# Kernel tuning notes

Measured on AMD Instinct MI355X. Metric: run time of the kernel, lower is better.

## Reference

```python
import jax, jax.numpy as jnp
import numpy as np

DIM = 256
HEADS = 8
HD = DIM // HEADS        # head_dim = 32
WS = 8                   # window_size (Wh = Ww = 8)
NEXP = 8                 # num_experts
HID = 128                # attr_hidden_size (router hidden)
SCALE = HD ** -0.5


def _window_partition(x, ws):
    # (B, H, W, C) -> (B * H//ws * W//ws, ws, ws, C)
    B, H, W, C = x.shape
    x = x.reshape(B, H // ws, ws, W // ws, ws, C)
    return x.transpose(0, 1, 3, 2, 4, 5).reshape(-1, ws, ws, C)


def _window_reverse(w, ws, B, H, W):
    # inverse of _window_partition
    C = w.shape[-1]
    x = w.reshape(B, H // ws, W // ws, ws, ws, C)
    return x.transpose(0, 1, 3, 2, 4, 5).reshape(B, H, W, C)


def _rope2(x):
    # 2D rotary embedding over a window: x (B*, Wh, Ww, d).
    # First d/2 channels rotated by row position, last d/2 by column position.
    B, Wh, Ww, d = x.shape
    d2 = d // 2

    def angles(L, dd):
        inv = 1.0 / (10000.0 ** (jnp.arange(0, dd, 2, dtype=jnp.float32) / dd))
        return jnp.arange(L, dtype=jnp.float32)[:, None] * inv[None, :]  # (L, dd//2)

    def rotate(v, ang, bshape):
        # v: (B, Wh, Ww, dd) pairs interleaved; ang broadcast as bshape
        p = v.reshape(*v.shape[:-1], -1, 2)
        c = jnp.cos(ang).reshape(bshape)
        s = jnp.sin(ang).reshape(bshape)
        o0 = p[..., 0] * c - p[..., 1] * s
        o1 = p[..., 0] * s + p[..., 1] * c
        return jnp.stack([o0, o1], axis=-1).reshape(v.shape)

    ah = angles(Wh, d2)  # (Wh, d2//2)
    aw = angles(Ww, d2)  # (Ww, d2//2)
    xh = rotate(x[..., :d2], ah, (1, Wh, 1, d2 // 2))
    xw = rotate(x[..., d2:], aw, (1, 1, Ww, d2 // 2))
    return jnp.concatenate([xh, xw], axis=-1)


def _moe_linear(xf, routes, w, b):
    # Top-1 dispatch: per-expert dense GEMM, masked select (jit-safe, static shapes).
    # xf: (T, in), routes: (T,) int, w: (E, out, in), b: (E, out)
    out = jnp.zeros((xf.shape[0], w.shape[1]), xf.dtype)
    for i in range(w.shape[0]):
        y = xf @ w[i].T + b[i]
        out = jnp.where((routes == i)[:, None], y, out)
    return out


def setup_inputs() -> dict:
    key = jax.random.key(0)
    ks = jax.random.split(key, 8)
    sc = 0.02
    return {
        "x": jax.random.normal(ks[0], (8, 64, 64, DIM), jnp.float32),
        "router_w1": jax.random.normal(ks[1], (HID, DIM), jnp.float32) * sc,
        "router_b1": jnp.zeros((HID,), jnp.float32),
        "router_w2": jax.random.normal(ks[2], (NEXP, HID), jnp.float32) * sc,
        "router_b2": jnp.zeros((NEXP,), jnp.float32),
        "qkv_w": jax.random.normal(ks[3], (NEXP, 3 * DIM, DIM), jnp.float32) * sc,
        "qkv_b": jnp.zeros((NEXP, 3 * DIM), jnp.float32),
        "proj_w": jax.random.normal(ks[4], (NEXP, DIM, DIM), jnp.float32) * sc,
        "proj_b": jnp.zeros((NEXP, DIM), jnp.float32),
    }


def reference(x, router_w1, router_b1, router_w2, router_b2,
              qkv_w, qkv_b, proj_w, proj_b):
    Bs, H, W, C = x.shape
    xf = x.reshape(-1, C)  # (T, C), T = Bs*H*W

    # --- Top-1 router (eval mode: no noise, no token dropping) ---
    h = jax.nn.relu(xf @ router_w1.T + router_b1)
    router_logits = h @ router_w2.T + router_b2          # (T, E)
    router_probs = jax.nn.softmax(router_logits, axis=-1)
    route_prob_max = jnp.max(router_probs, axis=-1)       # (T,)
    routes = jnp.argmax(router_probs, axis=-1)            # (T,)

    # --- per-expert QKV projection (grouped dispatch) ---
    qkv = _moe_linear(xf, routes, qkv_w, qkv_b)           # (T, 3C)
    qkv = qkv.reshape(Bs, H, W, 3 * C)

    # --- window partition (shift=0, dilated=1 -> no roll, mask=None) ---
    qw = _window_partition(qkv, WS).reshape(-1, WS * WS, 3 * C)
    B_, N, _ = qw.shape
    qkv5 = qw.reshape(B_, N, 3, HEADS, HD).transpose(2, 0, 3, 1, 4)  # (3,B_,h,N,hd)
    q, k, v = qkv5[0], qkv5[1], qkv5[2]

    # --- RoPE on q, k over the 2D window ---
    q = _rope2(q.reshape(-1, WS, WS, HD)).reshape(B_, HEADS, N, HD)
    k = _rope2(k.reshape(-1, WS, WS, HD)).reshape(B_, HEADS, N, HD)

    # --- windowed attention (moe_mask is all zeros in eval: no drops) ---
    attn = jax.nn.softmax((q * SCALE) @ k.swapaxes(-2, -1), axis=-1)  # (B_,h,N,N)
    out = (attn @ v).swapaxes(1, 2).reshape(B_, N, C)

    # --- window reverse ---
    out = _window_reverse(out.reshape(-1, WS, WS, C), WS, Bs, H, W)

    # --- per-expert output projection + Switch-style prob scaling ---
    of = _moe_linear(out.reshape(-1, C), routes, proj_w, proj_b)
    of = of * route_prob_max[:, None]
    return of.reshape(Bs, H, W, C)
```

## Files before the change

kernel.cpp:

```cpp
#include <hip/hip_runtime.h>
#include <hip/hip_bf16.h>

typedef unsigned short u16;
typedef unsigned int u32;
typedef __attribute__((ext_vector_type(8))) short short8;
typedef __attribute__((ext_vector_type(4))) float f32x4;

#define T_TOK 32768
#define SCALE_ATT 0.17677669529663687f

__device__ __forceinline__ u16 f2bf(float f){
  u32 u = __float_as_uint(f);
  u32 r = u + 0x7fffu + ((u >> 16) & 1u);
  return (u16)(r >> 16);
}
__device__ __forceinline__ float bf2f(u16 h){
  return __uint_as_float(((u32)h) << 16);
}

__global__ void k_cvt(const float* __restrict__ s, u16* __restrict__ d, int n4){
  int i = blockIdx.x * blockDim.x + threadIdx.x;
  if (i < n4){
    float4 v = ((const float4*)s)[i];
    ushort4 o;
    o.x = f2bf(v.x); o.y = f2bf(v.y); o.z = f2bf(v.z); o.w = f2bf(v.w);
    ((ushort4*)d)[i] = o;
  }
}

__global__ void k_cvt_split(const float* __restrict__ s, u16* __restrict__ hi,
                            u16* __restrict__ lo, int n){
  int i = blockIdx.x * blockDim.x + threadIdx.x;
  if (i < n){
    float v = s[i];
    u16 h = f2bf(v);
    hi[i] = h;
    lo[i] = f2bf(v - bf2f(h));
  }
}

__global__ void k_init(int* counts, int* cursors){
  int t = threadIdx.x;
  if (t < 8){ counts[t] = 0; cursors[t] = 0; }
}

__global__ __launch_bounds__(256) void k_router(
    const float* __restrict__ x, const u16* __restrict__ w1h, const u16* __restrict__ w1l,
    const float* __restrict__ b1, const float* __restrict__ w2, const float* __restrict__ b2,
    int* __restrict__ routes, float* __restrict__ pmax, int* __restrict__ counts,
    u16* __restrict__ x_bf)
{
  __shared__ __align__(16) char smem[64*132*4];
  u16* Ah = (u16*)smem;
  u16* Al = Ah + 2560;
  u16* Bh = Al + 2560;
  u16* Bl = Bh + 5120;
  float* Hs = (float*)smem;
  __shared__ int lhist[8];

  int tid = threadIdx.x;
  int t0 = blockIdx.x * 64;
  int wv = tid >> 6, lane = tid & 63, quad = lane >> 4, l16 = lane & 15;
  if (tid < 8) lhist[tid] = 0;

  int arow = tid >> 2, acg = tid & 3;
  int brow = tid >> 1, bhalf = tid & 1;

  f32x4 acc[4][2];
  #pragma unroll
  for (int i = 0; i < 4; ++i)
    #pragma unroll
    for (int j = 0; j < 2; ++j)
      #pragma unroll
      for (int rr = 0; rr < 4; ++rr) acc[i][j][rr] = 0.f;

  for (int kt = 0; kt < 8; ++kt){
    const float* gx = x + (size_t)(t0 + arow) * 256 + kt * 32 + acg * 8;
    float4 v0 = *(const float4*)gx;
    float4 v1 = *(const float4*)(gx + 4);
    ushort4 h0, h1, l0, l1;
    h0.x = f2bf(v0.x); h0.y = f2bf(v0.y); h0.z = f2bf(v0.z); h0.w = f2bf(v0.w);
    h1.x = f2bf(v1.x); h1.y = f2bf(v1.y); h1.z = f2bf(v1.z); h1.w = f2bf(v1.w);
    l0.x = f2bf(v0.x - bf2f(h0.x)); l0.y = f2bf(v0.y - bf2f(h0.y));
    l0.z = f2bf(v0.z - bf2f(h0.z)); l0.w = f2bf(v0.w - bf2f(h0.w));
    l1.x = f2bf(v1.x - bf2f(h1.x)); l1.y = f2bf(v1.y - bf2f(h1.y));
    l1.z = f2bf(v1.z - bf2f(h1.z)); l1.w = f2bf(v1.w - bf2f(h1.w));
    u16* gxb = x_bf + (size_t)(t0 + arow) * 256 + kt * 32 + acg * 8;
    *(ushort4*)gxb = h0; *(ushort4*)(gxb + 4) = h1;
    const u16* gwh = w1h + (size_t)brow * 256 + kt * 32 + bhalf * 16;
    const u16* gwl = w1l + (size_t)brow * 256 + kt * 32 + bhalf * 16;
    uint4 wh0 = *(const uint4*)gwh;
    uint4 wh1 = *(const uint4*)(gwh + 8);
    uint4 wl0 = *(const uint4*)gwl;
    uint4 wl1 = *(const uint4*)(gwl + 8);
    __syncthreads();
    *(ushort4*)&Ah[arow*40 + acg*8    ] = h0;
    *(ushort4*)&Ah[arow*40 + acg*8 + 4] = h1;
    *(ushort4*)&Al[arow*40 + acg*8    ] = l0;
    *(ushort4*)&Al[arow*40 + acg*8 + 4] = l1;
    *(uint4*)&Bh[brow*40 + bhalf*16    ] = wh0;
    *(uint4*)&Bh[brow*40 + bhalf*16 + 8] = wh1;
    *(uint4*)&Bl[brow*40 + bhalf*16    ] = wl0;
    *(uint4*)&Bl[brow*40 + bhalf*16 + 8] = wl1;
    __syncthreads();
    short8 ah[4], al[4], bhf[2], blf[2];
    #pragma unroll
    for (int i = 0; i < 4; ++i){
      ah[i] = *(const short8*)&Ah[(i*16 + l16)*40 + quad*8];
      al[i] = *(const short8*)&Al[(i*16 + l16)*40 + quad*8];
    }
    #pragma unroll
    for (int j = 0; j < 2; ++j){
      bhf[j] = *(const short8*)&Bh[(wv*32 + j*16 + l16)*40 + quad*8];
      blf[j] = *(const short8*)&Bl[(wv*32 + j*16 + l16)*40 + quad*8];
    }
    #pragma unroll
    for (int i = 0; i < 4; ++i)
      #pragma unroll
      for (int j = 0; j < 2; ++j){
        acc[i][j] = __builtin_amdgcn_mfma_f32_16x16x32_bf16(ah[i], bhf[j], acc[i][j], 0, 0, 0);
        acc[i][j] = __builtin_amdgcn_mfma_f32_16x16x32_bf16(ah[i], blf[j], acc[i][j], 0, 0, 0);
        acc[i][j] = __builtin_amdgcn_mfma_f32_16x16x32_bf16(al[i], bhf[j], acc[i][j], 0, 0, 0);
      }
  }
  __syncthreads();

  #pragma unroll
  for (int i = 0; i < 4; ++i)
    #pragma unroll
    for (int j = 0; j < 2; ++j){
      int col = wv*32 + j*16 + l16;
      float bb = b1[col];
      #pragma unroll
      for (int rr = 0; rr < 4; ++rr){
        float h = acc[i][j][rr] + bb;
        Hs[(i*16 + quad*4 + rr)*132 + col] = h > 0.f ? h : 0.f;
      }
    }
  __syncthreads();

  #pragma unroll
  for (int pass = 0; pass < 2; ++pass){
    int mtok = (tid >> 3) + pass * 32;
    int e = tid & 7;
    const float4* w2r = (const float4*)(w2 + e * 128);
    float l = b2[e];
    #pragma unroll
    for (int k4 = 0; k4 < 32; ++k4){
      float4 w = w2r[k4];
      int k = k4 * 4;
      l = fmaf(Hs[mtok*132+k  ], w.x, l);
      l = fmaf(Hs[mtok*132+k+1], w.y, l);
      l = fmaf(Hs[mtok*132+k+2], w.z, l);
      l = fmaf(Hs[mtok*132+k+3], w.w, l);
    }
    float mv = l; int mi = e;
    #pragma unroll
    for (int off = 1; off < 8; off <<= 1){
      float ov = __shfl_xor(mv, off, 64);
      int   oi = __shfl_xor(mi, off, 64);
      if (ov > mv || (ov == mv && oi < mi)){ mv = ov; mi = oi; }
    }
    float sum = expf(l - mv);
    #pragma unroll
    for (int off = 1; off < 8; off <<= 1) sum += __shfl_xor(sum, off, 64);
    if (e == 0){
      int t = t0 + mtok;
      routes[t] = mi;
      pmax[t] = 1.0f / sum;
      atomicAdd(&lhist[mi], 1);
    }
  }
  __syncthreads();
  if (tid < 8 && lhist[tid] > 0) atomicAdd(&counts[tid], lhist[tid]);
}

__global__ void k_offsets(const int* __restrict__ counts, int* __restrict__ offs,
                          int* __restrict__ sorted){
  __shared__ int so[9];
  if (threadIdx.x == 0){
    int o = 0; so[0] = 0;
    for (int e = 0; e < 8; ++e){ o += ((counts[e] + 127) >> 7) << 7; so[e+1] = o; }
    for (int e = 0; e < 9; ++e) offs[e] = so[e];
  }
  __syncthreads();
  for (int e = 0; e < 8; ++e){
    int s = so[e] + counts[e], en = so[e+1];
    for (int i = s + (int)threadIdx.x; i < en; i += (int)blockDim.x) sorted[i] = -1;
  }
}

__global__ __launch_bounds__(256) void k_scatter(
    const int* __restrict__ routes, const int* __restrict__ offs,
    int* __restrict__ cursors, int* __restrict__ sorted, int* __restrict__ rank)
{
  __shared__ int lc[8], lb[8];
  int tid = threadIdx.x;
  int t = blockIdx.x * 256 + tid;
  if (tid < 8) lc[tid] = 0;
  __syncthreads();
  int e = routes[t];
  int rl = atomicAdd(&lc[e], 1);
  __syncthreads();
  if (tid < 8 && lc[tid] > 0) lb[tid] = atomicAdd(&cursors[tid], lc[tid]);
  __syncthreads();
  int pos = offs[e] + lb[e] + rl;
  sorted[pos] = t;
  rank[t] = pos;
}

__global__ __launch_bounds__(256) void k_gather(
    const u16* __restrict__ xbf, const int* __restrict__ sorted,
    const int* __restrict__ offs, u16* __restrict__ xs)
{
  int total = offs[8];
  int tid = threadIdx.x;
  #pragma unroll
  for (int h = 0; h < 2; ++h){
    int cid = tid + h * 256;
    int row = cid >> 5, chunk = cid & 31;
    int gr = blockIdx.x * 16 + row;
    int t = (gr < total) ? sorted[gr] : -1;
    uint4 v = {0u, 0u, 0u, 0u};
    if (t >= 0) v = *(const uint4*)(xbf + (size_t)t * 256 + chunk * 8);
    *(uint4*)(xs + (size_t)gr * 256 + chunk * 8) = v;
  }
}

#define ASTR 56
template<int NOUT, bool PROJ>
__global__ __launch_bounds__(256) void k_gemm(
    const u16* __restrict__ A, const u16* __restrict__ W,
    const float* __restrict__ bias, const int* __restrict__ sidx,
    const int* __restrict__ offs, const float* __restrict__ pmax,
    u16* __restrict__ outb, float* __restrict__ outf)
{
  __shared__ __align__(16) u16 As[128 * ASTR];
  __shared__ __align__(16) u16 Bs[128 * ASTR];
  int tid = threadIdx.x;
  int m0 = blockIdx.y * 128;
  int n0 = blockIdx.x * 128;
  int total = offs[8];
  if (m0 >= total) return;
  int e = 0;
  #pragma unroll
  for (int i = 1; i < 8; ++i) if (m0 >= offs[i]) e = i;

  int wv = tid >> 6, lane = tid & 63, quad = lane >> 4, l16 = lane & 15;
  int wrow = (wv >> 1) * 64, wcol = (wv & 1) * 64;

  int row0 = tid >> 2, c0 = tid & 3;
  const u16* aptr0 = A + (size_t)(m0 + row0) * 256 + c0 * 8;
  const u16* aptr1 = aptr0 + (size_t)64 * 256;
  int pc = (row0 >> 4) + (row0 & 15) * 4;
  const u16* bptr0 = W + ((size_t)e * NOUT + n0 + pc) * 256 + c0 * 8;
  const u16* bptr1 = W + ((size_t)e * NOUT + n0 + 64 + pc) * 256 + c0 * 8;

  f32x4 acc[4][4];
  #pragma unroll
  for (int i = 0; i < 4; ++i)
    #pragma unroll
    for (int j = 0; j < 4; ++j)
      #pragma unroll
      for (int r = 0; r < 4; ++r) acc[i][j][r] = 0.f;

  uint4 a0 = *(const uint4*)aptr0, a1 = *(const uint4*)aptr1;
  uint4 b0 = *(const uint4*)bptr0, b1 = *(const uint4*)bptr1;

  for (int kt = 0; kt < 8; ++kt){
    __syncthreads();
    *(uint4*)&As[ row0      *ASTR + c0*8] = a0;
    *(uint4*)&As[(row0 + 64)*ASTR + c0*8] = a1;
    *(uint4*)&Bs[ row0      *ASTR + c0*8] = b0;
    *(uint4*)&Bs[(row0 + 64)*ASTR + c0*8] = b1;
    __syncthreads();
    if (kt < 7){
      a0 = *(const uint4*)(aptr0 + (kt+1)*32);
      a1 = *(const uint4*)(aptr1 + (kt+1)*32);
      b0 = *(const uint4*)(bptr0 + (kt+1)*32);
      b1 = *(const uint4*)(bptr1 + (kt+1)*32);
    }
    short8 af[4], bfv[4];
    #pragma unroll
    for (int i = 0; i < 4; ++i)
      af[i] = *(const short8*)&As[(wrow + i*16 + l16)*ASTR + quad*8];
    #pragma unroll
    for (int j = 0; j < 4; ++j)
      bfv[j] = *(const short8*)&Bs[(wcol + j*16 + l16)*ASTR + quad*8];
    #pragma unroll
    for (int i = 0; i < 4; ++i)
      #pragma unroll
      for (int j = 0; j < 4; ++j)
        acc[i][j] = __builtin_amdgcn_mfma_f32_16x16x32_bf16(af[i], bfv[j], acc[i][j], 0, 0, 0);
  }

  float4 bj4 = *(const float4*)&bias[e*NOUT + n0 + wcol + l16*4];
  #pragma unroll
  for (int i = 0; i < 4; ++i){
    #pragma unroll
    for (int ri = 0; ri < 4; ++ri){
      int row = wrow + i*16 + quad*4 + ri;
      int t = sidx[m0 + row];
      if (t < 0) continue;
      if (PROJ){
        float pm = pmax[t];
        float4 ov;
        ov.x = (acc[i][0][ri] + bj4.x) * pm;
        ov.y = (acc[i][1][ri] + bj4.y) * pm;
        ov.z = (acc[i][2][ri] + bj4.z) * pm;
        ov.w = (acc[i][3][ri] + bj4.w) * pm;
        *(float4*)&outf[(size_t)t * NOUT + n0 + wcol + l16*4] = ov;
      } else {
        uint2 ov;
        ov.x = (u32)f2bf(acc[i][0][ri] + bj4.x) | ((u32)f2bf(acc[i][1][ri] + bj4.y) << 16);
        ov.y = (u32)f2bf(acc[i][2][ri] + bj4.z) | ((u32)f2bf(acc[i][3][ri] + bj4.w) << 16);
        *(uint2*)&outb[(size_t)t * NOUT + n0 + wcol + l16*4] = ov;
      }
    }
  }
}

__global__ __launch_bounds__(128) void k_attn(const u16* __restrict__ qkv,
                                              const int* __restrict__ rank,
                                              u16* __restrict__ attn_s)
{
  __shared__ __align__(16) u16 lds[2][8576];
  int tid = threadIdx.x;
  int w = tid >> 6, lane = tid & 63;
  u16* Qs = &lds[w][0];
  u16* Ks = &lds[w][2560];
  u16* Ps = &lds[w][0];
  u16* Vt = &lds[w][5120];

  int wh = blockIdx.x * 2 + w;
  if (wh >= 4096) return;
  int win = wh >> 3, head = wh & 7;
  int b = win >> 6, wy = (win >> 3) & 7, wx = win & 7;
  int r = lane >> 3, c = lane & 7;
  int tn = b * 4096 + (wy*8 + r) * 64 + (wx*8 + c);
  const u16* base = qkv + (size_t)tn * 768 + head * 32;

  uint4 qa[4], ka[4], va[4];
  #pragma unroll
  for (int i = 0; i < 4; ++i){
    qa[i] = ((const uint4*)(base      ))[i];
    ka[i] = ((const uint4*)(base + 256))[i];
    va[i] = ((const uint4*)(base + 512))[i];
  }
  u32* qu = (u32*)qa; u32* ku = (u32*)ka; u32* vu = (u32*)va;

  #pragma unroll
  for (int j = 0; j < 8; ++j){
    float inv = __expf(-1.1512925465f * (float)j);
    float ah = (float)r * inv, aw = (float)c * inv;
    float ch = cosf(ah), sh = sinf(ah), cw = cosf(aw), sw = sinf(aw);
    u32 v0, v1; float a0, b0;
    v0 = qu[j];   a0 = bf2f((u16)(v0 & 0xffff)); b0 = bf2f((u16)(v0 >> 16));
    qu[j]   = (u32)f2bf(a0*ch - b0*sh) | ((u32)f2bf(a0*sh + b0*ch) << 16);
    v1 = qu[8+j]; a0 = bf2f((u16)(v1 & 0xffff)); b0 = bf2f((u16)(v1 >> 16));
    qu[8+j] = (u32)f2bf(a0*cw - b0*sw) | ((u32)f2bf(a0*sw + b0*cw) << 16);
    v0 = ku[j];   a0 = bf2f((u16)(v0 & 0xffff)); b0 = bf2f((u16)(v0 >> 16));
    ku[j]   = (u32)f2bf(a0*ch - b0*sh) | ((u32)f2bf(a0*sh + b0*ch) << 16);
    v1 = ku[8+j]; a0 = bf2f((u16)(v1 & 0xffff)); b0 = bf2f((u16)(v1 >> 16));
    ku[8+j] = (u32)f2bf(a0*cw - b0*sw) | ((u32)f2bf(a0*sw + b0*cw) << 16);
  }

  #pragma unroll
  for (int i = 0; i < 4; ++i){
    *(uint4*)&Qs[lane*40 + i*8] = qa[i];
    *(uint4*)&Ks[lane*40 + i*8] = ka[i];
  }
  int pn = (lane & 15) * 4 + (lane >> 4);
  #pragma unroll
  for (int d2 = 0; d2 < 16; ++d2){
    Vt[(2*d2  )*72 + pn] = (u16)(vu[d2] & 0xffff);
    Vt[(2*d2+1)*72 + pn] = (u16)(vu[d2] >> 16);
  }
  uint4 ones = {0x3F803F80u, 0x3F803F80u, 0x3F803F80u, 0x3F803F80u};
  *(uint4*)&Vt[(32 + (lane >> 3))*72 + (lane & 7)*8] = ones;
  *(uint4*)&Vt[(40 + (lane >> 3))*72 + (lane & 7)*8] = ones;

  int quad = lane >> 4, l16 = lane & 15;

  short8 qf[4], kf[4];
  #pragma unroll
  for (int i = 0; i < 4; ++i) qf[i] = *(const short8*)&Qs[(i*16 + l16)*40 + quad*8];
  #pragma unroll
  for (int j = 0; j < 4; ++j) kf[j] = *(const short8*)&Ks[(j*16 + l16)*40 + quad*8];

  f32x4 sa[4][4];
  #pragma unroll
  for (int i = 0; i < 4; ++i)
    #pragma unroll
    for (int j = 0; j < 4; ++j){
      #pragma unroll
      for (int rr = 0; rr < 4; ++rr) sa[i][j][rr] = 0.f;
      sa[i][j] = __builtin_amdgcn_mfma_f32_16x16x32_bf16(qf[i], kf[j], sa[i][j], 0, 0, 0);
    }

  #pragma unroll
  for (int i = 0; i < 4; ++i)
    #pragma unroll
    for (int rr = 0; rr < 4; ++rr){
      float e0 = __expf(sa[i][0][rr] * SCALE_ATT);
      float e1 = __expf(sa[i][1][rr] * SCALE_ATT);
      float e2 = __expf(sa[i][2][rr] * SCALE_ATT);
      float e3 = __expf(sa[i][3][rr] * SCALE_ATT);
      uint2 pk;
      pk.x = (u32)f2bf(e0) | ((u32)f2bf(e1) << 16);
      pk.y = (u32)f2bf(e2) | ((u32)f2bf(e3) << 16);
      *(uint2*)&Ps[(i*16 + quad*4 + rr)*72 + l16*4] = pk;
    }

  f32x4 oa[4][2], os[4];
  #pragma unroll
  for (int i = 0; i < 4; ++i){
    #pragma unroll
    for (int rr = 0; rr < 4; ++rr){ oa[i][0][rr] = 0.f; oa[i][1][rr] = 0.f; os[i][rr] = 0.f; }
  }
  #pragma unroll
  for (int ks = 0; ks < 2; ++ks){
    short8 vf0 = *(const short8*)&Vt[(     l16)*72 + ks*32 + quad*8];
    short8 vf1 = *(const short8*)&Vt[(16 + l16)*72 + ks*32 + quad*8];
    short8 vf2 = *(const short8*)&Vt[(32 + l16)*72 + ks*32 + quad*8];
    #pragma unroll
    for (int i = 0; i < 4; ++i){
      short8 pf = *(const short8*)&Ps[(i*16 + l16)*72 + ks*32 + quad*8];
      oa[i][0] = __builtin_amdgcn_mfma_f32_16x16x32_bf16(pf, vf0, oa[i][0], 0, 0, 0);
      oa[i][1] = __builtin_amdgcn_mfma_f32_16x16x32_bf16(pf, vf1, oa[i][1], 0, 0, 0);
      os[i]    = __builtin_amdgcn_mfma_f32_16x16x32_bf16(pf, vf2, os[i],    0, 0, 0);
    }
  }

  int tb = b * 4096 + wy * 512 + wx * 8;
  #pragma unroll
  for (int i = 0; i < 4; ++i)
    #pragma unroll
    for (int rr = 0; rr < 4; ++rr){
      float inv = __builtin_amdgcn_rcpf(os[i][rr]);
      int m = i*16 + quad*4 + rr;
      int tm = tb + (m >> 3) * 64 + (m & 7);
      int pos = rank[tm];
      u16* op = attn_s + (size_t)pos * 256 + head * 32 + l16;
      op[0]  = f2bf(oa[i][0][rr] * inv);
      op[16] = f2bf(oa[i][1][rr] * inv);
    }
}

extern "C" void kernel_launch(void* const* d_in, const int* in_sizes, int n_in,
                              void* d_out, int out_size, void* d_ws, size_t ws_size,
                              hipStream_t stream){
  const float* x     = (const float*)d_in[0];
  const float* rw1   = (const float*)d_in[1];
  const float* rb1   = (const float*)d_in[2];
  const float* rw2   = (const float*)d_in[3];
  const float* rb2   = (const float*)d_in[4];
  const float* qkvw  = (const float*)d_in[5];
  const float* qkvb  = (const float*)d_in[6];
  const float* projw = (const float*)d_in[7];
  const float* projb = (const float*)d_in[8];
  float* out = (float*)d_out;

  char* ws = (char*)d_ws;
  u16*   x_bf    = (u16*)(ws);
  u16*   qkv_bf  = (u16*)(ws + 16777216);
  u16*   w1h     = (u16*)(ws + 67108864);
  u16*   w1l     = w1h + 32768;
  u16*   xs      = (u16*)(ws + 67108864);
  u16*   attn_s  = (u16*)(ws + 67108864);
  u16*   qw_bf   = (u16*)(ws + 84410368);
  u16*   pw_bf   = (u16*)(ws + 87556096);
  int*   routes  = (int*)(ws + 88604672);
  float* pmaxp   = (float*)(ws + 88735744);
  int*   sorted  = (int*)(ws + 88866816);
  int*   rank    = (int*)(ws + 89001984);
  int*   counts  = (int*)(ws + 89133056);
  int*   cursors = (int*)(ws + 89133056 + 32);
  int*   offs    = (int*)(ws + 89133056 + 64);

  k_init<<<1, 64, 0, stream>>>(counts, cursors);
  k_cvt<<<1536, 256, 0, stream>>>(qkvw,  qw_bf, 1572864/4);
  k_cvt<<< 512, 256, 0, stream>>>(projw, pw_bf,  524288/4);
  k_cvt_split<<<128, 256, 0, stream>>>(rw1, w1h, w1l, 32768);
  k_router<<<512, 256, 0, stream>>>(x, w1h, w1l, rb1, rw2, rb2, routes, pmaxp, counts, x_bf);
  k_offsets<<<1, 256, 0, stream>>>(counts, offs, sorted);
  k_scatter<<<128, 256, 0, stream>>>(routes, offs, cursors, sorted, rank);
  k_gather<<<2112, 256, 0, stream>>>(x_bf, sorted, offs, xs);
  k_gemm<768, false><<<dim3(6, 264), 256, 0, stream>>>(xs, qw_bf, qkvb, sorted, offs,
                                                       nullptr, qkv_bf, nullptr);
  k_attn<<<2048, 128, 0, stream>>>(qkv_bf, rank, attn_s);
  k_gemm<256, true><<<dim3(2, 264), 256, 0, stream>>>(attn_s, pw_bf, projb, sorted, offs,
                                                      pmaxp, nullptr, out);
}
```

Measured before the change: 224.7 us.

## Fuse RoPE and q scaling into QKV GEMM epilogue, slim attention kernel

```diff
diff --git a/kernel.cpp b/kernel.cpp
--- a/kernel.cpp
+++ b/kernel.cpp
@@ -295,14 +295,14 @@
   }
 
   float4 bj4 = *(const float4*)&bias[e*NOUT + n0 + wcol + l16*4];
-  #pragma unroll
-  for (int i = 0; i < 4; ++i){
-    #pragma unroll
-    for (int ri = 0; ri < 4; ++ri){
-      int row = wrow + i*16 + quad*4 + ri;
-      int t = sidx[m0 + row];
-      if (t < 0) continue;
-      if (PROJ){
+  if (PROJ){
+    #pragma unroll
+    for (int i = 0; i < 4; ++i){
+      #pragma unroll
+      for (int ri = 0; ri < 4; ++ri){
+        int row = wrow + i*16 + quad*4 + ri;
+        int t = sidx[m0 + row];
+        if (t < 0) continue;
         float pm = pmax[t];
         float4 ov;
         ov.x = (acc[i][0][ri] + bj4.x) * pm;
@@ -310,83 +310,77 @@
         ov.z = (acc[i][2][ri] + bj4.z) * pm;
         ov.w = (acc[i][3][ri] + bj4.w) * pm;
         *(float4*)&outf[(size_t)t * NOUT + n0 + wcol + l16*4] = ov;
-      } else {
+      }
+    }
+  } else {
+    int col0 = n0 + wcol + l16*4;
+    bool isqk = (col0 < 512);
+    float inv0 = 0.f, inv1 = 0.f;
+    float qsc = (col0 < 256) ? SCALE_ATT : 1.0f;
+    if (isqk){
+      int p0 = (col0 & 15) >> 1;
+      inv0 = __expf(-1.1512925465f * (float)p0);
+      inv1 = inv0 * 0.31622776601683794f;
+    }
+    #pragma unroll
+    for (int i = 0; i < 4; ++i){
+      #pragma unroll
+      for (int ri = 0; ri < 4; ++ri){
+        int row = wrow + i*16 + quad*4 + ri;
+        int t = sidx[m0 + row];
+        if (t < 0) continue;
+        float vx = acc[i][0][ri] + bj4.x;
+        float vy = acc[i][1][ri] + bj4.y;
+        float vz = acc[i][2][ri] + bj4.z;
+        float vw = acc[i][3][ri] + bj4.w;
+        if (isqk){
+          float pos = (float)((col0 & 16) ? (t & 7) : ((t >> 6) & 7));
+          float a0 = pos * inv0, a1 = pos * inv1;
+          float s0, c0s, s1, c1s;
+          __sincosf(a0, &s0, &c0s);
+          __sincosf(a1, &s1, &c1s);
+          float r0 = (vx*c0s - vy*s0) * qsc;
+          float r1 = (vx*s0 + vy*c0s) * qsc;
+          float r2 = (vz*c1s - vw*s1) * qsc;
+          float r3 = (vz*s1 + vw*c1s) * qsc;
+          vx = r0; vy = r1; vz = r2; vw = r3;
+        }
         uint2 ov;
-        ov.x = (u32)f2bf(acc[i][0][ri] + bj4.x) | ((u32)f2bf(acc[i][1][ri] + bj4.y) << 16);
-        ov.y = (u32)f2bf(acc[i][2][ri] + bj4.z) | ((u32)f2bf(acc[i][3][ri] + bj4.w) << 16);
+        ov.x = (u32)f2bf(vx) | ((u32)f2bf(vy) << 16);
+        ov.y = (u32)f2bf(vz) | ((u32)f2bf(vw) << 16);
         *(uint2*)&outb[(size_t)t * NOUT + n0 + wcol + l16*4] = ov;
       }
     }
   }
 }
 
-__global__ __launch_bounds__(128) void k_attn(const u16* __restrict__ qkv,
-                                              const int* __restrict__ rank,
-                                              u16* __restrict__ attn_s)
+__global__ __launch_bounds__(64, 3) void k_attn(const u16* __restrict__ qkv,
+                                                const int* __restrict__ rank,
+                                                u16* __restrict__ attn_s)
 {
-  __shared__ __align__(16) u16 lds[2][8576];
-  int tid = threadIdx.x;
-  int w = tid >> 6, lane = tid & 63;
-  u16* Qs = &lds[w][0];
-  u16* Ks = &lds[w][2560];
-  u16* Ps = &lds[w][0];
-  u16* Vt = &lds[w][5120];
-
-  int wh = blockIdx.x * 2 + w;
-  if (wh >= 4096) return;
+  __shared__ __align__(16) u16 Ps[64*72];
+  __shared__ __align__(16) u16 Vt[32*72];
+
+  int lane = threadIdx.x;
+  int quad = lane >> 4, l16 = lane & 15;
+  int wh = blockIdx.x;
   int win = wh >> 3, head = wh & 7;
   int b = win >> 6, wy = (win >> 3) & 7, wx = win & 7;
-  int r = lane >> 3, c = lane & 7;
-  int tn = b * 4096 + (wy*8 + r) * 64 + (wx*8 + c);
-  const u16* base = qkv + (size_t)tn * 768 + head * 32;
-
-  uint4 qa[4], ka[4], va[4];
+  int tb = b*4096 + wy*512 + wx*8;
+
+  short8 qf[4], kf[4];
   #pragma unroll
   for (int i = 0; i < 4; ++i){
-    qa[i] = ((const uint4*)(base      ))[i];
-    ka[i] = ((const uint4*)(base + 256))[i];
-    va[i] = ((const uint4*)(base + 512))[i];
-  }
-  u32* qu = (u32*)qa; u32* ku = (u32*)ka; u32* vu = (u32*)va;
-
-  #pragma unroll
-  for (int j = 0; j < 8; ++j){
-    float inv = __expf(-1.1512925465f * (float)j);
-    float ah = (float)r * inv, aw = (float)c * inv;
-    float ch = cosf(ah), sh = sinf(ah), cw = cosf(aw), sw = sinf(aw);
-    u32 v0, v1; float a0, b0;
-    v0 = qu[j];   a0 = bf2f((u16)(v0 & 0xffff)); b0 = bf2f((u16)(v0 >> 16));
-    qu[j]   = (u32)f2bf(a0*ch - b0*sh) | ((u32)f2bf(a0*sh + b0*ch) << 16);
-    v1 = qu[8+j]; a0 = bf2f((u16)(v1 & 0xffff)); b0 = bf2f((u16)(v1 >> 16));
-    qu[8+j] = (u32)f2bf(a0*cw - b0*sw) | ((u32)f2bf(a0*sw + b0*cw) << 16);
-    v0 = ku[j];   a0 = bf2f((u16)(v0 & 0xffff)); b0 = bf2f((u16)(v0 >> 16));
-    ku[j]   = (u32)f2bf(a0*ch - b0*sh) | ((u32)f2bf(a0*sh + b0*ch) << 16);
-    v1 = ku[8+j]; a0 = bf2f((u16)(v1 & 0xffff)); b0 = bf2f((u16)(v1 >> 16));
-    ku[8+j] = (u32)f2bf(a0*cw - b0*sw) | ((u32)f2bf(a0*sw + b0*cw) << 16);
-  }
-
-  #pragma unroll
-  for (int i = 0; i < 4; ++i){
-    *(uint4*)&Qs[lane*40 + i*8] = qa[i];
-    *(uint4*)&Ks[lane*40 + i*8] = ka[i];
-  }
-  int pn = (lane & 15) * 4 + (lane >> 4);
-  #pragma unroll
-  for (int d2 = 0; d2 < 16; ++d2){
-    Vt[(2*d2  )*72 + pn] = (u16)(vu[d2] & 0xffff);
-    Vt[(2*d2+1)*72 + pn] = (u16)(vu[d2] >> 16);
-  }
-  uint4 ones = {0x3F803F80u, 0x3F803F80u, 0x3F803F80u, 0x3F803F80u};
-  *(uint4*)&Vt[(32 + (lane >> 3))*72 + (lane & 7)*8] = ones;
-  *(uint4*)&Vt[(40 + (lane >> 3))*72 + (lane & 7)*8] = ones;
-
-  int quad = lane >> 4, l16 = lane & 15;
-
-  short8 qf[4], kf[4];
-  #pragma unroll
-  for (int i = 0; i < 4; ++i) qf[i] = *(const short8*)&Qs[(i*16 + l16)*40 + quad*8];
-  #pragma unroll
-  for (int j = 0; j < 4; ++j) kf[j] = *(const short8*)&Ks[(j*16 + l16)*40 + quad*8];
+    int n = i*16 + l16;
+    const u16* p = qkv + (size_t)(tb + (n>>3)*64 + (n&7)) * 768 + head*32 + quad*8;
+    qf[i] = *(const short8*)p;
+    kf[i] = *(const short8*)(p + 256);
+  }
+  int tn = tb + (lane>>3)*64 + (lane&7);
+  const uint4* vb = (const uint4*)(qkv + (size_t)tn * 768 + 512 + head*32);
+  uint4 va[4];
+  #pragma unroll
+  for (int i = 0; i < 4; ++i) va[i] = vb[i];
 
   f32x4 sa[4][4];
   #pragma unroll
@@ -398,46 +392,60 @@
       sa[i][j] = __builtin_amdgcn_mfma_f32_16x16x32_bf16(qf[i], kf[j], sa[i][j], 0, 0, 0);
     }
 
+  f32x4 rs[4];
   #pragma unroll
   for (int i = 0; i < 4; ++i)
     #pragma unroll
     for (int rr = 0; rr < 4; ++rr){
-      float e0 = __expf(sa[i][0][rr] * SCALE_ATT);
-      float e1 = __expf(sa[i][1][rr] * SCALE_ATT);
-      float e2 = __expf(sa[i][2][rr] * SCALE_ATT);
-      float e3 = __expf(sa[i][3][rr] * SCALE_ATT);
+      float e0 = __expf(sa[i][0][rr]);
+      float e1 = __expf(sa[i][1][rr]);
+      float e2 = __expf(sa[i][2][rr]);
+      float e3 = __expf(sa[i][3][rr]);
+      rs[i][rr] = (e0 + e1) + (e2 + e3);
       uint2 pk;
       pk.x = (u32)f2bf(e0) | ((u32)f2bf(e1) << 16);
       pk.y = (u32)f2bf(e2) | ((u32)f2bf(e3) << 16);
       *(uint2*)&Ps[(i*16 + quad*4 + rr)*72 + l16*4] = pk;
     }
-
-  f32x4 oa[4][2], os[4];
-  #pragma unroll
-  for (int i = 0; i < 4; ++i){
-    #pragma unroll
-    for (int rr = 0; rr < 4; ++rr){ oa[i][0][rr] = 0.f; oa[i][1][rr] = 0.f; os[i][rr] = 0.f; }
-  }
+  #pragma unroll
+  for (int i = 0; i < 4; ++i)
+    #pragma unroll
+    for (int rr = 0; rr < 4; ++rr){
+      #pragma unroll
+      for (int off = 1; off < 16; off <<= 1)
+        rs[i][rr] += __shfl_xor(rs[i][rr], off, 64);
+    }
+
+  u32* vu = (u32*)va;
+  int pn = l16 * 4 + quad;
+  #pragma unroll
+  for (int d2 = 0; d2 < 16; ++d2){
+    Vt[(2*d2  )*72 + pn] = (u16)(vu[d2] & 0xffff);
+    Vt[(2*d2+1)*72 + pn] = (u16)(vu[d2] >> 16);
+  }
+
+  f32x4 oa[4][2];
+  #pragma unroll
+  for (int i = 0; i < 4; ++i)
+    #pragma unroll
+    for (int rr = 0; rr < 4; ++rr){ oa[i][0][rr] = 0.f; oa[i][1][rr] = 0.f; }
   #pragma unroll
   for (int ks = 0; ks < 2; ++ks){
     short8 vf0 = *(const short8*)&Vt[(     l16)*72 + ks*32 + quad*8];
     short8 vf1 = *(const short8*)&Vt[(16 + l16)*72 + ks*32 + quad*8];
-    short8 vf2 = *(const short8*)&Vt[(32 + l16)*72 + ks*32 + quad*8];
     #pragma unroll
     for (int i = 0; i < 4; ++i){
       short8 pf = *(const short8*)&Ps[(i*16 + l16)*72 + ks*32 + quad*8];
       oa[i][0] = __builtin_amdgcn_mfma_f32_16x16x32_bf16(pf, vf0, oa[i][0], 0, 0, 0);
       oa[i][1] = __builtin_amdgcn_mfma_f32_16x16x32_bf16(pf, vf1, oa[i][1], 0, 0, 0);
-      os[i]    = __builtin_amdgcn_mfma_f32_16x16x32_bf16(pf, vf2, os[i],    0, 0, 0);
-    }
-  }
-
-  int tb = b * 4096 + wy * 512 + wx * 8;
+    }
+  }
+
   #pragma unroll
   for (int i = 0; i < 4; ++i)
     #pragma unroll
     for (int rr = 0; rr < 4; ++rr){
-      float inv = __builtin_amdgcn_rcpf(os[i][rr]);
+      float inv = __builtin_amdgcn_rcpf(rs[i][rr]);
       int m = i*16 + quad*4 + rr;
       int tm = tb + (m >> 3) * 64 + (m & 7);
       int pos = rank[tm];
@@ -488,7 +496,7 @@
   k_gather<<<2112, 256, 0, stream>>>(x_bf, sorted, offs, xs);
   k_gemm<768, false><<<dim3(6, 264), 256, 0, stream>>>(xs, qw_bf, qkvb, sorted, offs,
                                                        nullptr, qkv_bf, nullptr);
-  k_attn<<<2048, 128, 0, stream>>>(qkv_bf, rank, attn_s);
+  k_attn<<<4096, 64, 0, stream>>>(qkv_bf, rank, attn_s);
   k_gemm<256, true><<<dim3(2, 264), 256, 0, stream>>>(attn_s, pw_bf, projb, sorted, offs,
                                                       pmaxp, nullptr, out);
 }
```

Result: no change. 224.6 us (-0.0%).
